# Optimization experiments

Measured on AMD Instinct MI355X. Metric: run time of the kernel, lower is better.

## Reference

```python
import jax, jax.numpy as jnp
import numpy as np

H = W = 64            # grid resolution (input image HxW)
N = H * W
T = 25                # landscape sample points
K_MAX = 2             # landscape levels
M0 = 0.05             # DTM mass parameter
LIMS = [[224.0, 0.0], [0.0, 224.0]]
T_MIN, T_MAX = 0.0, 45.0   # fixed tseq covering the DTM value range for this grid scale


def _grid_coords():
    gx = np.linspace(LIMS[0][0], LIMS[0][1], H)
    gy = np.linspace(LIMS[1][0], LIMS[1][1], W)
    X, Y = np.meshgrid(gx, gy, indexing='ij')
    return np.stack([X.ravel(), Y.ravel()], 1).astype(np.float32)  # [N,2]


def _grid_edges():
    idx = np.arange(N).reshape(H, W)
    e_h = np.stack([idx[:, :-1].ravel(), idx[:, 1:].ravel()], 1)
    e_v = np.stack([idx[:-1, :].ravel(), idx[1:, :].ravel()], 1)
    return np.concatenate([e_h, e_v], 0).astype(np.int32)  # [E,2] 4-connectivity


def dtm(w):
    """Weighted (robust) distance-to-measure on the fixed grid, r=2. w: [B,N] >=0."""
    coords = jnp.asarray(_grid_coords())
    diff = coords[:, None, :] - coords[None, :, :]
    d2 = jnp.sum(diff * diff, -1)                      # [N,N] squared distances
    idx = jnp.argsort(d2, axis=1)                      # fixed nearest-neighbor order
    d2s = jnp.take_along_axis(d2, idx, axis=1)         # [N,N]
    wsort = w[:, idx]                                  # [B,N,N] weights in distance order
    cumw = jnp.cumsum(wsort, -1)
    thr = M0 * jnp.sum(w, -1)[:, None, None]           # [B,1,1] target mass
    # fractional mass contribution of each neighbor until cumulative mass hits thr
    eff = jnp.clip(thr - (cumw - wsort), 0.0, wsort)
    return jnp.sqrt(jnp.sum(eff * d2s, -1) / thr[..., 0])  # [B,N]


def ph0(f, edges):
    """0-dim sublevel persistence of vertex function f on the grid graph (elder rule)."""
    u, v = edges[:, 0], edges[:, 1]
    wgt = jnp.maximum(f[u], f[v])          # edge filtration values
    es = edges[jnp.argsort(wgt)]

    def step(label, e):
        eu, ev = e[0], e[1]
        ru, rv = label[eu], label[ev]
        bu, bv = f[ru], f[rv]
        u_elder = (bu < bv) | ((bu == bv) & (ru <= rv))
        elder = jnp.where(u_elder, ru, rv)
        younger = jnp.where(u_elder, rv, ru)
        merge = ru != rv
        birth = f[younger]
        death = jnp.maximum(f[eu], f[ev])
        label = jnp.where(merge & (label == younger), elder, label)
        return label, (birth, death, merge)

    label0 = jnp.arange(N, dtype=jnp.int32)
    _, (b, d, valid) = jax.lax.scan(step, label0, es)
    # essential class: global min, killed at max filtration value
    b = jnp.concatenate([b, f.min()[None]])
    d = jnp.concatenate([d, f.max()[None]])
    valid = jnp.concatenate([valid, jnp.array([True])])
    return b, d, valid


def landscape(b, d, valid, tseq):
    # tent functions: [P,T]
    tri = jnp.minimum(tseq[None, :] - b[:, None], d[:, None] - tseq[None, :])
    tri = jnp.where(valid[:, None], jnp.maximum(tri, 0.0), 0.0)
    top = jax.lax.top_k(tri.T, K_MAX)[0]   # [T, K_MAX]
    return top.T.reshape(-1)               # [K_MAX*T]


def reference(input, Wg, bg, Wfc, bfc):
    B = input.shape[0]
    w = input.reshape(B, -1)               # Flatten: pixel weights on the grid
    f = dtm(w)                             # [B,N] DTM filtration
    edges = jnp.asarray(_grid_edges())
    b, d, valid = jax.vmap(lambda fi: ph0(fi, edges))(f)
    tseq = jnp.linspace(T_MIN, T_MAX, T, dtype=jnp.float32)
    land = jax.vmap(lambda bi, di, vi: landscape(bi, di, vi, tseq))(b, d, valid)  # [B,50]
    x = land @ Wg.T + bg                   # learned g_theta -> out_features
    signal = jnp.abs(jax.lax.stop_gradient(x)).sum(0)
    output = jnp.maximum(x, 0.0) @ Wfc.T + bfc
    return output, signal


def setup_inputs() -> dict:
    key = jax.random.key(0)
    k1, k2, k3 = jax.random.split(key, 3)
    B = 2
    return {
        'input': jax.random.uniform(k1, (B, 1, H, W), dtype=jnp.float32),
        'Wg': 0.1 * jax.random.normal(k2, (50, K_MAX * T), dtype=jnp.float32),
        'bg': jnp.zeros((50,), jnp.float32),
        'Wfc': 0.1 * jax.random.normal(k3, (10, 50), dtype=jnp.float32),
        'bfc': jnp.zeros((10,), jnp.float32),
    }
```

## Files before the change

### kernel.cpp

```cpp
#include <hip/hip_runtime.h>

#define NPTS 4096
#define NEDGE 8064
#define M0f 0.05f
#define KMAXD2 7938
#define IDCAP 90
#define SORTCAP 512
#define PAIRCAP 160

typedef unsigned long long u64;

__device__ inline float waveSum(float x) {
  for (int m = 32; m >= 1; m >>= 1) x += __shfl_xor(x, m);
  return x;
}

__device__ inline int isqrt_i(int x) {
  int r = (int)sqrtf((float)x);
  if ((r + 1) * (r + 1) <= x) r++;
  else if (r * r > x) r--;
  return r;
}

__device__ inline int rdl(int v, int l) { return __builtin_amdgcn_readlane(v, l); }
__device__ inline float rdlf(float v, int l) {
  return __uint_as_float((unsigned)__builtin_amdgcn_readlane((int)__float_as_uint(v), l));
}
__device__ inline u64 rdl64(u64 x, int l) {
  unsigned lo = (unsigned)__builtin_amdgcn_readlane((int)(unsigned)(x & 0xffffffffull), l);
  unsigned hi = (unsigned)__builtin_amdgcn_readlane((int)(unsigned)(x >> 32), l);
  return ((u64)hi << 32) | (u64)lo;
}
__device__ inline int sel2(int v0, int v1, int idx) {
  int x0 = __shfl(v0, idx & 63);
  int x1 = __shfl(v1, idx & 63);
  return (idx < 64) ? x0 : x1;
}
__device__ inline u64 shfl_xor64(u64 x, int m) {
  int lo = __shfl_xor((int)(unsigned)(x & 0xffffffffull), m);
  int hi = __shfl_xor((int)(unsigned)(x >> 32), m);
  return ((u64)(unsigned)hi << 32) | (u64)(unsigned)lo;
}

#define CXL(R, J, K) { \
  u64 vo = shfl_xor64(e##R, J); \
  bool up = (((((R) * 64) & (K)) | (lane & (K))) == 0); \
  bool lower = ((lane & (J)) == 0); \
  bool kmin = (lower == up); \
  u64 mn = (e##R < vo) ? e##R : vo; \
  u64 mx = (e##R < vo) ? vo : e##R; \
  e##R = kmin ? mn : mx; }
#define ALL2(J, K) CXL(0,J,K) CXL(1,J,K)
#define CXR(RA, RB, K) { \
  const bool up = ((((RA) * 64) & (K)) == 0); \
  u64 va = e##RA, vb = e##RB; \
  u64 mn = (va < vb) ? va : vb; \
  u64 mx = (va < vb) ? vb : va; \
  e##RA = up ? mn : mx; e##RB = up ? mx : mn; }

__global__ __launch_bounds__(1024) void dtm_kernel(const float* __restrict__ win,
                                                   float* __restrict__ fout,
                                                   float* __restrict__ out) {
  __shared__ float P0[64][65];
  __shared__ float P1[64][65];
  __shared__ float P2[64][65];
  int b = blockIdx.y;
  const float* w = win + b * NPTS;
  int tid = threadIdx.x, lane = tid & 63, wv = tid >> 6;

  if (blockIdx.x == 0 && blockIdx.y == 0 && tid < 50) out[20 + tid] = 0.f;

  for (int rr = 0; rr < 4; ++rr) {
    int r = (wv << 2) | rr;
    float x0 = w[(r << 6) | lane];
    float fl = (float)lane;
    float x1 = x0 * fl, x2 = x1 * fl;
    for (int d = 1; d < 64; d <<= 1) {
      float t0 = __shfl_up(x0, d);
      float t1 = __shfl_up(x1, d);
      float t2 = __shfl_up(x2, d);
      if (lane >= d) { x0 += t0; x1 += t1; x2 += t2; }
    }
    P0[r][lane] = x0; P1[r][lane] = x1; P2[r][lane] = x2;
  }
  __syncthreads();

  float sumw = waveSum(P0[lane][63]);
  float thr = M0f * sumw;

  int q = blockIdx.x * 16 + wv;
  int qi = q >> 6, qj = q & 63;
  int di = qi - lane;
  int disq = di * di;

  auto evalF = [&](int K) -> float {
    float s0 = 0.f;
    int rem = K - disq;
    if (rem >= 0) {
      int r = isqrt_i(rem);
      int l0 = qj - r; l0 = l0 < 0 ? 0 : l0;
      int h0 = qj + r; h0 = h0 > 63 ? 63 : h0;
      s0 = P0[lane][h0] - (l0 > 0 ? P0[lane][l0 - 1] : 0.f);
    }
    return waveSum(s0);
  };

  int lo = -1, hi = 256;
  float Flo = 0.f;
  for (;;) {
    float F = evalF(hi);
    if (F >= thr || hi == KMAXD2) break;
    lo = hi; Flo = F;
    hi = (hi == 256) ? 1024 : KMAXD2;
  }
  while (hi - lo > 1) {
    int mid = (lo + hi) >> 1;
    float F = evalF(mid);
    if (F >= thr) hi = mid; else { lo = mid; Flo = F; }
  }
  int kstar = hi;
  float Fm = Flo;

  float g = 0.f;
  {
    int rem = (kstar - 1) - disq;
    if (rem >= 0) {
      int r = isqrt_i(rem);
      int l0 = qj - r; l0 = l0 < 0 ? 0 : l0;
      int h0 = qj + r; h0 = h0 > 63 ? 63 : h0;
      float S0 = P0[lane][h0] - (l0 > 0 ? P0[lane][l0 - 1] : 0.f);
      float S1 = P1[lane][h0] - (l0 > 0 ? P1[lane][l0 - 1] : 0.f);
      float S2 = P2[lane][h0] - (l0 > 0 ? P2[lane][l0 - 1] : 0.f);
      float fq = (float)qj;
      g = (float)disq * S0 + fq * fq * S0 - 2.f * fq * S1 + S2;
    }
  }
  float G = waveSum(g);
  float val = (G + (thr - Fm) * (float)kstar) / thr;
  val = val < 0.f ? 0.f : val;
  float res = (224.f / 63.f) * sqrtf(val);
  if (lane == 0) fout[b * NPTS + q] = res;
}

__global__ __launch_bounds__(1024) void ph_fused(const float* __restrict__ fin,
                                                 const float* __restrict__ Wg,
                                                 const float* __restrict__ bg,
                                                 const float* __restrict__ Wfc,
                                                 const float* __restrict__ bfc,
                                                 float* __restrict__ out) {
  __shared__ __align__(16) float sf[NPTS];
  __shared__ __align__(16) int srep[NPTS];
  __shared__ __align__(16) int sbasin[NPTS];
  __shared__ float smu[128];
  __shared__ int sminv[128];
  __shared__ float2 spairs[PAIRCAP];
  __shared__ float sland[50];
  __shared__ float sx[50];
  __shared__ __align__(16) float sWg[2500];
  __shared__ float sbg[50];
  __shared__ __align__(16) float sWfc[500];
  __shared__ float sbfc[10];
  __shared__ int comparr[128];
  __shared__ u64 minKey[128];
  __shared__ u64 mstlist[128];
  __shared__ int c_m, c_np, c_hook, c_chg;
  __shared__ unsigned fminb, fmaxb;
  __shared__ int c_l2;

  int b = blockIdx.x;
  int tid = threadIdx.x;
  int lane = tid & 63;
  if (tid == 0) { c_m = 0; c_l2 = 0; c_np = 0; c_chg = 0; fminb = 0x7f800000u; fmaxb = 0u; }
  if (tid < 128) { smu[tid] = 3.0e38f; sminv[tid] = tid; mstlist[tid] = ~0ull; }

  if (tid < 625) ((float4*)sWg)[tid] = ((const float4*)Wg)[tid];
  if (tid < 125) ((float4*)sWfc)[tid] = ((const float4*)Wfc)[tid];
  if (tid < 50) sbg[tid] = bg[tid];
  if (tid >= 64 && tid < 74) sbfc[tid - 64] = bfc[tid - 64];

  {
    float4 v4 = ((const float4*)(fin + b * NPTS))[tid];
    ((float4*)sf)[tid] = v4;
    float lmin = fminf(fminf(v4.x, v4.y), fminf(v4.z, v4.w));
    float lmax = fmaxf(fmaxf(v4.x, v4.y), fmaxf(v4.z, v4.w));
    for (int m = 32; m >= 1; m >>= 1) {
      lmin = fminf(lmin, __shfl_xor(lmin, m));
      lmax = fmaxf(lmax, __shfl_xor(lmax, m));
    }
    if (lane == 0) {
      atomicMin(&fminb, __float_as_uint(lmin));
      atomicMax(&fmaxb, __float_as_uint(lmax));
    }
  }
  __syncthreads();

  int preg[4];
#pragma unroll 4
  for (int s = 0; s < 4; ++s) {
    int v = tid + s * 1024;
    int vi = v >> 6, vj = v & 63;
    float bf = sf[v]; int bi = v;
    if (vj > 0)  { float fn = sf[v - 1];  int n = v - 1;  if (fn < bf || (fn == bf && n < bi)) { bf = fn; bi = n; } }
    if (vj < 63) { float fn = sf[v + 1];  int n = v + 1;  if (fn < bf || (fn == bf && n < bi)) { bf = fn; bi = n; } }
    if (vi > 0)  { float fn = sf[v - 64]; int n = v - 64; if (fn < bf || (fn == bf && n < bi)) { bf = fn; bi = n; } }
    if (vi < 63) { float fn = sf[v + 64]; int n = v + 64; if (fn < bf || (fn == bf && n < bi)) { bf = fn; bi = n; } }
    srep[v] = bi;
    preg[s] = bi;
  }
  __syncthreads();

  for (int it = 0; it < 8; ++it) {
    bool ch = false;
#pragma unroll 4
    for (int s = 0; s < 4; ++s) {
      int x = srep[preg[s]];
      x = srep[x];
      ch |= (x != preg[s]);
      srep[tid + s * 1024] = x;
      preg[s] = x;
    }
    u64 bl = __ballot(ch);
    if (lane == 0 && bl != 0ull) c_chg = it + 1;
    __syncthreads();
    if (c_chg != it + 1) break;
  }

  for (int v = tid; v < NPTS; v += 1024) {
    if (srep[v] == v) {
      int id = atomicAdd(&c_m, 1);
      if (id < IDCAP) { sbasin[v] = id; smu[id] = sf[v]; sminv[id] = v; }
      else sbasin[v] = IDCAP - 1;
    }
  }
  __syncthreads();
  for (int v = tid; v < NPTS; v += 1024) {
    if (srep[v] != v) sbasin[v] = sbasin[srep[v]];
  }
  __syncthreads();

  unsigned* ptable = (unsigned*)srep;
  for (int i = tid; i < 4096; i += 1024) ptable[i] = 0xFFFFFFFFu;
  __syncthreads();
  for (int e = tid; e < NEDGE; e += 1024) {
    int u, v2;
    if (e < 4032) { int i = e / 63; int j = e - i * 63; u = (i << 6) | j; v2 = u + 1; }
    else          { int e2 = e - 4032; u = e2; v2 = u + 64; }
    int bu = sbasin[u], bv = sbasin[v2];
    if (bu != bv) {
      float wgt = fmaxf(sf[u], sf[v2]);
      int a = bu < bv ? bu : bv, bb2 = bu < bv ? bv : bu;
      int t = (bb2 * (bb2 - 1)) / 2 + a;
      atomicMin(&ptable[t], __float_as_uint(wgt));
    }
  }
  __syncthreads();

  u64* slist2 = (u64*)sbasin;
  for (int t = tid; t < 4096; t += 1024) {
    unsigned wv2 = ptable[t];
    if (wv2 != 0xFFFFFFFFu) {
      int bb2 = (int)((1.0f + sqrtf(1.0f + 8.0f * (float)t)) * 0.5f);
      while (bb2 > 1 && (bb2 * (bb2 - 1)) / 2 > t) bb2--;
      while (((bb2 + 1) * bb2) / 2 <= t) bb2++;
      int aa = t - (bb2 * (bb2 - 1)) / 2;
      int slot = atomicAdd(&c_l2, 1);
      if (slot < SORTCAP) slist2[slot] = ((u64)wv2 << 32) | (unsigned)((bb2 << 8) | aa);
    }
  }
  __syncthreads();
  int n2 = c_l2; if (n2 > SORTCAP) n2 = SORTCAP;

  int comp0 = lane, comp1 = 64 + lane;
  int nmst = 0;
  for (int round = 0; round < 7; ++round) {
    if (tid < 64) {
      comparr[lane] = comp0; comparr[64 + lane] = comp1;
      if (lane == 0) c_hook = 0;
    }
    if (tid < 128) minKey[tid] = ~0ull;
    __syncthreads();
    for (int e = tid; e < n2; e += 1024) {
      u64 ev = slist2[e];
      int a = (int)(ev & 0xffull), bb2 = (int)((ev >> 8) & 0xffull);
      int ra = comparr[a], rb = comparr[bb2];
      if (ra != rb) {
        u64 key = (ev & 0xFFFFFFFF00000000ull) | (u64)(unsigned)e;
        atomicMin(&minKey[ra], key);
        atomicMin(&minKey[rb], key);
      }
    }
    __syncthreads();
    if (tid < 64) {
      u64 k0 = minKey[lane], k1 = minKey[64 + lane];
      unsigned mi0 = (k0 != ~0ull) ? (unsigned)(k0 & 0xffffffffull) : 0xFFFFFFFFu;
      unsigned mi1 = (k1 != ~0ull) ? (unsigned)(k1 & 0xffffffffull) : 0xFFFFFFFFu;
      u64 ev0 = (mi0 != 0xFFFFFFFFu) ? slist2[mi0] : 0ull;
      u64 ev1 = (mi1 != 0xFFFFFFFFu) ? slist2[mi1] : 0ull;
      int a0 = (int)(ev0 & 0xffull), b0 = (int)((ev0 >> 8) & 0xffull);
      int a1 = (int)(ev1 & 0xffull), b1 = (int)((ev1 >> 8) & 0xffull);
      int raA = sel2(comp0, comp1, a0), rbA = sel2(comp0, comp1, b0);
      int raB = sel2(comp0, comp1, a1), rbB = sel2(comp0, comp1, b1);
      int parA0 = (mi0 != 0xFFFFFFFFu) ? ((raA == lane) ? rbA : raA) : lane;
      int parA1 = (mi1 != 0xFFFFFFFFu) ? ((raB == 64 + lane) ? rbB : raB) : (64 + lane);
      int pp0 = sel2(parA0, parA1, parA0);
      int pp1 = sel2(parA0, parA1, parA1);
      int par0 = (pp0 == lane && lane < parA0) ? lane : parA0;
      int par1 = (pp1 == (64 + lane) && (64 + lane) < parA1) ? (64 + lane) : parA1;
      bool h0 = (par0 != lane);
      bool h1 = (par1 != (64 + lane));
      u64 mlo = __ballot(h0);
      int cnt0 = __popcll(mlo);
      int pos0 = nmst + __popcll(mlo & ((1ull << lane) - 1ull));
      if (h0 && pos0 < 128) mstlist[pos0] = ev0;
      u64 mhi = __ballot(h1);
      int pos1 = nmst + cnt0 + __popcll(mhi & ((1ull << lane) - 1ull));
      if (h1 && pos1 < 128) mstlist[pos1] = ev1;
      int tot = cnt0 + __popcll(mhi);
      nmst += tot;
      if (lane == 0 && tot > 0) c_hook = 1;
      for (int j = 0; j < 7; ++j) {
        int n0 = sel2(par0, par1, par0);
        int n1 = sel2(par0, par1, par1);
        bool chp = (n0 != par0) || (n1 != par1);
        par0 = n0; par1 = n1;
        if (__ballot(chp) == 0ull) break;
      }
      comp0 = sel2(par0, par1, comp0);
      comp1 = sel2(par0, par1, comp1);
    }
    __syncthreads();
    if (c_hook == 0) break;
  }

  if (tid < 64) {
    u64 e0 = mstlist[lane], e1 = mstlist[64 + lane];
    ALL2(1,2)
    ALL2(2,4) ALL2(1,4)
    ALL2(4,8) ALL2(2,8) ALL2(1,8)
    ALL2(8,16) ALL2(4,16) ALL2(2,16) ALL2(1,16)
    ALL2(16,32) ALL2(8,32) ALL2(4,32) ALL2(2,32) ALL2(1,32)
    ALL2(32,64) ALL2(16,64) ALL2(8,64) ALL2(4,64) ALL2(2,64) ALL2(1,64)
    CXR(0,1,128)
    ALL2(32,128) ALL2(16,128) ALL2(8,128) ALL2(4,128) ALL2(2,128) ALL2(1,128)

    int p0 = lane, p1 = 64 + lane;
    float m0 = smu[lane], m1 = smu[64 + lane];
    int r0 = sminv[lane], r1 = sminv[64 + lane];
    int np = 0;
    for (int s = 0; s < nmst; ++s) {
      u64 ev = (s < 64) ? rdl64(e0, s) : rdl64(e1, s - 64);
      int a = (int)(ev & 0xffull), bb2 = (int)((ev >> 8) & 0xffull);
      unsigned wb = (unsigned)(ev >> 32);
      int ia = a & 63, ib = bb2 & 63;
      int pa = (a < 64) ? rdl(p0, ia) : rdl(p1, ia);
      int pb = (bb2 < 64) ? rdl(p0, ib) : rdl(p1, ib);
      if (pa == pb) continue;
      float ma = (a < 64) ? rdlf(m0, ia) : rdlf(m1, ia);
      float mb = (bb2 < 64) ? rdlf(m0, ib) : rdlf(m1, ib);
      int ra = (a < 64) ? rdl(r0, ia) : rdl(r1, ia);
      int rb = (bb2 < 64) ? rdl(r0, ib) : rdl(r1, ib);
      bool aeld = (ma < mb) || (ma == mb && ra <= rb);
      int eld = aeld ? pa : pb, yng = aeld ? pb : pa;
      float m_e = aeld ? ma : mb; int r_e = aeld ? ra : rb;
      float byoung = aeld ? mb : ma;
      bool g0 = (p0 == yng), g1 = (p1 == yng);
      p0 = g0 ? eld : p0; m0 = g0 ? m_e : m0; r0 = g0 ? r_e : r0;
      p1 = g1 ? eld : p1; m1 = g1 ? m_e : m1; r1 = g1 ? r_e : r1;
      if (lane == 0 && np < PAIRCAP - 1) spairs[np] = make_float2(byoung, __uint_as_float(wb));
      np++;
    }
    if (np > PAIRCAP - 1) np = PAIRCAP - 1;
    if (lane == 0) {
      spairs[np] = make_float2(__uint_as_float(fminb), __uint_as_float(fmaxb));
      c_np = np + 1;
    }
  }
  __syncthreads();

  int totp = c_np;
  if (tid < 25) {
    float tv = 1.875f * (float)tid;
    float top1 = 0.f, top2 = 0.f;
    for (int i = 0; i < totp; ++i) {
      float2 p = spairs[i];
      float tri = fminf(tv - p.x, p.y - tv);
      tri = fmaxf(tri, 0.f);
      if (tri > top1) { top2 = top1; top1 = tri; }
      else if (tri > top2) top2 = tri;
    }
    sland[tid] = top1;
    sland[25 + tid] = top2;
  }
  __syncthreads();

  if (tid < 50) {
    float acc = sbg[tid];
    for (int k = 0; k < 50; ++k) acc += sland[k] * sWg[tid * 50 + k];
    sx[tid] = acc;
  }
  __syncthreads();

  if (tid < 50) atomicAdd(&out[20 + tid], fabsf(sx[tid]));
  if (tid >= 64 && tid < 74) {
    int c = tid - 64;
    float acc = sbfc[c];
    for (int o = 0; o < 50; ++o) acc += fmaxf(sx[o], 0.f) * sWfc[c * 50 + o];
    out[b * 10 + c] = acc;
  }
}

extern "C" void kernel_launch(void* const* d_in, const int* in_sizes, int n_in,
                              void* d_out, int out_size, void* d_ws, size_t ws_size,
                              hipStream_t stream) {
  (void)in_sizes; (void)n_in; (void)out_size; (void)ws_size;
  const float* input = (const float*)d_in[0];
  const float* Wg  = (const float*)d_in[1];
  const float* bg  = (const float*)d_in[2];
  const float* Wfc = (const float*)d_in[3];
  const float* bfc = (const float*)d_in[4];
  float* out = (float*)d_out;

  float* f_ws = (float*)d_ws;

  dtm_kernel<<<dim3(256, 2), 1024, 0, stream>>>(input, f_ws, out);
  ph_fused<<<dim3(2), 1024, 0, stream>>>(f_ws, Wg, bg, Wfc, bfc, out);
}
```

Baseline: 62.85 us.

## Use interpolation search for DTM radius, pack union-find state, widen MST list

The DTM radius search now runs over the full range, alternating interpolation steps (using the bracketing cumulative masses) with bisection steps, instead of galloping and then bisecting. The goal is fewer wave-wide prefix-sum evaluations per query. In the single-wave merge phase, each component's parent, birth value and min index are packed into one 64-bit key, so each step needs fewer readlanes and a single elder comparison. The MST edge list grows from 128 to 256 entries, which adds a larger bitonic sort stage. The interpolation search can take more iterations when the mass distribution is badly skewed, and the bigger sort costs extra instructions.

```diff
diff --git a/kernel.cpp b/kernel.cpp
--- a/kernel.cpp
+++ b/kernel.cpp
@@ -7,6 +7,7 @@
 #define IDCAP 90
 #define SORTCAP 512
 #define PAIRCAP 160
+#define MSTCAP 256
 
 typedef unsigned long long u64;
 
@@ -23,9 +24,6 @@
 }
 
 __device__ inline int rdl(int v, int l) { return __builtin_amdgcn_readlane(v, l); }
-__device__ inline float rdlf(float v, int l) {
-  return __uint_as_float((unsigned)__builtin_amdgcn_readlane((int)__float_as_uint(v), l));
-}
 __device__ inline u64 rdl64(u64 x, int l) {
   unsigned lo = (unsigned)__builtin_amdgcn_readlane((int)(unsigned)(x & 0xffffffffull), l);
   unsigned hi = (unsigned)__builtin_amdgcn_readlane((int)(unsigned)(x >> 32), l);
@@ -50,7 +48,7 @@
   u64 mn = (e##R < vo) ? e##R : vo; \
   u64 mx = (e##R < vo) ? vo : e##R; \
   e##R = kmin ? mn : mx; }
-#define ALL2(J, K) CXL(0,J,K) CXL(1,J,K)
+#define ALL4(J, K) CXL(0,J,K) CXL(1,J,K) CXL(2,J,K) CXL(3,J,K)
 #define CXR(RA, RB, K) { \
   const bool up = ((((RA) * 64) & (K)) == 0); \
   u64 va = e##RA, vb = e##RB; \
@@ -105,18 +103,21 @@
     return waveSum(s0);
   };
 
-  int lo = -1, hi = 256;
-  float Flo = 0.f;
-  for (;;) {
-    float F = evalF(hi);
-    if (F >= thr || hi == KMAXD2) break;
-    lo = hi; Flo = F;
-    hi = (hi == 256) ? 1024 : KMAXD2;
-  }
-  while (hi - lo > 1) {
-    int mid = (lo + hi) >> 1;
+  int lo = -1, hi = KMAXD2;
+  float Flo = 0.f, Fhi = sumw;
+  int itc = 0;
+  while (hi - lo > 1 && itc < 40) {
+    int mid;
+    if (itc & 1) {
+      mid = (lo + hi) >> 1;
+    } else {
+      float t = (thr - Flo) / fmaxf(Fhi - Flo, 1e-30f);
+      mid = lo + (int)(t * (float)(hi - lo));
+      mid = mid < lo + 1 ? lo + 1 : (mid > hi - 1 ? hi - 1 : mid);
+    }
     float F = evalF(mid);
-    if (F >= thr) hi = mid; else { lo = mid; Flo = F; }
+    if (F >= thr) { hi = mid; Fhi = F; } else { lo = mid; Flo = F; }
+    ++itc;
   }
   int kstar = hi;
   float Fm = Flo;
@@ -162,7 +163,7 @@
   __shared__ float sbfc[10];
   __shared__ int comparr[128];
   __shared__ u64 minKey[128];
-  __shared__ u64 mstlist[128];
+  __shared__ u64 mstlist[MSTCAP];
   __shared__ int c_m, c_np, c_hook, c_chg;
   __shared__ unsigned fminb, fmaxb;
   __shared__ int c_l2;
@@ -171,7 +172,8 @@
   int tid = threadIdx.x;
   int lane = tid & 63;
   if (tid == 0) { c_m = 0; c_l2 = 0; c_np = 0; c_chg = 0; fminb = 0x7f800000u; fmaxb = 0u; }
-  if (tid < 128) { smu[tid] = 3.0e38f; sminv[tid] = tid; mstlist[tid] = ~0ull; }
+  if (tid < 128) { smu[tid] = 3.0e38f; sminv[tid] = tid; }
+  if (tid < MSTCAP) mstlist[tid] = ~0ull;
 
   if (tid < 625) ((float4*)sWg)[tid] = ((const float4*)Wg)[tid];
   if (tid < 125) ((float4*)sWfc)[tid] = ((const float4*)Wfc)[tid];
@@ -311,10 +313,10 @@
       u64 mlo = __ballot(h0);
       int cnt0 = __popcll(mlo);
       int pos0 = nmst + __popcll(mlo & ((1ull << lane) - 1ull));
-      if (h0 && pos0 < 128) mstlist[pos0] = ev0;
+      if (h0 && pos0 < MSTCAP) mstlist[pos0] = ev0;
       u64 mhi = __ballot(h1);
       int pos1 = nmst + cnt0 + __popcll(mhi & ((1ull << lane) - 1ull));
-      if (h1 && pos1 < 128) mstlist[pos1] = ev1;
+      if (h1 && pos1 < MSTCAP) mstlist[pos1] = ev1;
       int tot = cnt0 + __popcll(mhi);
       nmst += tot;
       if (lane == 0 && tot > 0) c_hook = 1;
@@ -331,44 +333,47 @@
     __syncthreads();
     if (c_hook == 0) break;
   }
+  if (nmst > MSTCAP) nmst = MSTCAP;
 
   if (tid < 64) {
-    u64 e0 = mstlist[lane], e1 = mstlist[64 + lane];
-    ALL2(1,2)
-    ALL2(2,4) ALL2(1,4)
-    ALL2(4,8) ALL2(2,8) ALL2(1,8)
-    ALL2(8,16) ALL2(4,16) ALL2(2,16) ALL2(1,16)
-    ALL2(16,32) ALL2(8,32) ALL2(4,32) ALL2(2,32) ALL2(1,32)
-    ALL2(32,64) ALL2(16,64) ALL2(8,64) ALL2(4,64) ALL2(2,64) ALL2(1,64)
-    CXR(0,1,128)
-    ALL2(32,128) ALL2(16,128) ALL2(8,128) ALL2(4,128) ALL2(2,128) ALL2(1,128)
-
-    int p0 = lane, p1 = 64 + lane;
-    float m0 = smu[lane], m1 = smu[64 + lane];
-    int r0 = sminv[lane], r1 = sminv[64 + lane];
+    u64 e0 = mstlist[lane], e1 = mstlist[64 + lane], e2 = mstlist[128 + lane], e3 = mstlist[192 + lane];
+    ALL4(1,2)
+    ALL4(2,4) ALL4(1,4)
+    ALL4(4,8) ALL4(2,8) ALL4(1,8)
+    ALL4(8,16) ALL4(4,16) ALL4(2,16) ALL4(1,16)
+    ALL4(16,32) ALL4(8,32) ALL4(4,32) ALL4(2,32) ALL4(1,32)
+    ALL4(32,64) ALL4(16,64) ALL4(8,64) ALL4(4,64) ALL4(2,64) ALL4(1,64)
+    CXR(0,1,128) CXR(2,3,128)
+    ALL4(32,128) ALL4(16,128) ALL4(8,128) ALL4(4,128) ALL4(2,128) ALL4(1,128)
+    CXR(0,2,256) CXR(1,3,256)
+    CXR(0,1,256) CXR(2,3,256)
+    ALL4(32,256) ALL4(16,256) ALL4(8,256) ALL4(4,256) ALL4(2,256) ALL4(1,256)
+
+    u64 st0 = ((u64)__float_as_uint(smu[lane]) << 32) | ((u64)(unsigned)sminv[lane] << 13) | (unsigned)lane;
+    u64 st1 = ((u64)__float_as_uint(smu[64 + lane]) << 32) | ((u64)(unsigned)sminv[64 + lane] << 13) | (unsigned)(64 + lane);
     int np = 0;
-    for (int s = 0; s < nmst; ++s) {
-      u64 ev = (s < 64) ? rdl64(e0, s) : rdl64(e1, s - 64);
-      int a = (int)(ev & 0xffull), bb2 = (int)((ev >> 8) & 0xffull);
-      unsigned wb = (unsigned)(ev >> 32);
-      int ia = a & 63, ib = bb2 & 63;
-      int pa = (a < 64) ? rdl(p0, ia) : rdl(p1, ia);
-      int pb = (bb2 < 64) ? rdl(p0, ib) : rdl(p1, ib);
-      if (pa == pb) continue;
-      float ma = (a < 64) ? rdlf(m0, ia) : rdlf(m1, ia);
-      float mb = (bb2 < 64) ? rdlf(m0, ib) : rdlf(m1, ib);
-      int ra = (a < 64) ? rdl(r0, ia) : rdl(r1, ia);
-      int rb = (bb2 < 64) ? rdl(r0, ib) : rdl(r1, ib);
-      bool aeld = (ma < mb) || (ma == mb && ra <= rb);
-      int eld = aeld ? pa : pb, yng = aeld ? pb : pa;
-      float m_e = aeld ? ma : mb; int r_e = aeld ? ra : rb;
-      float byoung = aeld ? mb : ma;
-      bool g0 = (p0 == yng), g1 = (p1 == yng);
-      p0 = g0 ? eld : p0; m0 = g0 ? m_e : m0; r0 = g0 ? r_e : r0;
-      p1 = g1 ? eld : p1; m1 = g1 ? m_e : m1; r1 = g1 ? r_e : r1;
-      if (lane == 0 && np < PAIRCAP - 1) spairs[np] = make_float2(byoung, __uint_as_float(wb));
-      np++;
-    }
+#define KBLK(R, BASE) \
+    for (int s = 0; s < 64; ++s) { \
+      if (BASE + s >= nmst) break; \
+      u64 ev = rdl64(e##R, s); \
+      int a = (int)(ev & 0xffull), bb2 = (int)((ev >> 8) & 0xffull); \
+      int ia = a & 63, ib = bb2 & 63; \
+      u64 stA = (a < 64) ? rdl64(st0, ia) : rdl64(st1, ia); \
+      u64 stB = (bb2 < 64) ? rdl64(st0, ib) : rdl64(st1, ib); \
+      int pa = (int)(stA & 127ull), pb = (int)(stB & 127ull); \
+      if (pa == pb) continue; \
+      bool aeld = (stA >> 13) < (stB >> 13); \
+      u64 stE = aeld ? stA : stB; \
+      u64 stY = aeld ? stB : stA; \
+      unsigned yng = (unsigned)(stY & 127ull); \
+      float byoung = __uint_as_float((unsigned)(stY >> 32)); \
+      bool g0 = ((unsigned)(st0 & 127ull) == yng); st0 = g0 ? stE : st0; \
+      bool g1 = ((unsigned)(st1 & 127ull) == yng); st1 = g1 ? stE : st1; \
+      if (lane == 0 && np < PAIRCAP - 1) spairs[np] = make_float2(byoung, __uint_as_float((unsigned)(ev >> 32))); \
+      np++; \
+    }
+    KBLK(0, 0) KBLK(1, 64) KBLK(2, 128) KBLK(3, 192)
+#undef KBLK
     if (np > PAIRCAP - 1) np = PAIRCAP - 1;
     if (lane == 0) {
       spairs[np] = make_float2(__uint_as_float(fminb), __uint_as_float(fmaxb));
```

Result: faster. 58.29 us (-7.3%).
